# Kernel tuning notes

Hardware: AMD Instinct MI355X
Metric: run time of the kernel (lower is better)

Reference implementation:

```python
import jax, jax.numpy as jnp
import numpy as np

HEADS = 56
OUT = 32       # hidden_channels (per-head out dim)
N_FEAT = 128
N_CLASS = 2
N_NODES = 20000
N_EDGES = 100000
N_GRAPHS = 50
EPS_BN = 1e-5


def _gat_conv(x, W, att_src, att_dst, bias, src, dst, n, concat):
    # x: [n, in]; W: [in, H*O]; att_*: [H, O]
    h = (x @ W).reshape(n, HEADS, OUT)                     # [n, H, O]
    a_s = jnp.sum(h * att_src, axis=-1)                    # [n, H]
    a_d = jnp.sum(h * att_dst, axis=-1)                    # [n, H]
    e = jax.nn.leaky_relu(a_s[src] + a_d[dst], 0.2)        # [E, H]
    m = jax.ops.segment_max(e, dst, num_segments=n)        # per-dst max
    ex = jnp.exp(e - m[dst])
    den = jax.ops.segment_sum(ex, dst, num_segments=n)
    alpha = ex / den[dst]                                  # segment softmax over incoming edges
    msg = h[src] * alpha[:, :, None]                       # [E, H, O]
    out = jax.ops.segment_sum(msg, dst, num_segments=n)    # [n, H, O]
    if concat:
        return out.reshape(n, HEADS * OUT) + bias
    return out.mean(axis=1) + bias


def _bn_eval(x, gamma, beta, mean, var):
    return (x - mean) * jax.lax.rsqrt(var + EPS_BN) * gamma + beta


def setup_inputs() -> dict:
    key = jax.random.key(0)
    ks = jax.random.split(key, 20)
    d1 = HEADS * OUT
    inp = {
        'x': jax.random.normal(ks[0], (N_NODES, N_FEAT), jnp.float32),
        'edge_index': jax.random.randint(ks[1], (2, N_EDGES), 0, N_NODES, jnp.int32),
        'batch': jnp.sort(jax.random.randint(ks[2], (N_NODES,), 0, N_GRAPHS, jnp.int32)),
        'W1': jax.random.normal(ks[3], (N_FEAT, d1), jnp.float32) * (1.0 / np.sqrt(N_FEAT)),
        'att_src1': jax.random.normal(ks[4], (HEADS, OUT), jnp.float32) * 0.1,
        'att_dst1': jax.random.normal(ks[5], (HEADS, OUT), jnp.float32) * 0.1,
        'b1': jnp.zeros((d1,), jnp.float32),
        'bn1_g': jnp.ones((d1,), jnp.float32),
        'bn1_b': jnp.zeros((d1,), jnp.float32),
        'bn1_m': jax.random.normal(ks[6], (d1,), jnp.float32) * 0.1,
        'bn1_v': jax.random.uniform(ks[7], (d1,), jnp.float32) + 0.5,
        'W2': jax.random.normal(ks[8], (d1, d1), jnp.float32) * (1.0 / np.sqrt(d1)),
        'att_src2': jax.random.normal(ks[9], (HEADS, OUT), jnp.float32) * 0.1,
        'att_dst2': jax.random.normal(ks[10], (HEADS, OUT), jnp.float32) * 0.1,
        'b2': jnp.zeros((OUT,), jnp.float32),
        'bn2_g': jnp.ones((OUT,), jnp.float32),
        'bn2_b': jnp.zeros((OUT,), jnp.float32),
        'bn2_m': jax.random.normal(ks[11], (OUT,), jnp.float32) * 0.1,
        'bn2_v': jax.random.uniform(ks[12], (OUT,), jnp.float32) + 0.5,
        'lin_w': jax.random.normal(ks[13], (OUT, N_CLASS), jnp.float32) * (1.0 / np.sqrt(OUT)),
        'lin_b': jnp.zeros((N_CLASS,), jnp.float32),
    }
    return inp


def reference(x, edge_index, batch, W1, att_src1, att_dst1, b1, bn1_g, bn1_b, bn1_m, bn1_v,
              W2, att_src2, att_dst2, b2, bn2_g, bn2_b, bn2_m, bn2_v, lin_w, lin_b):
    n = x.shape[0]
    loop = jnp.arange(n, dtype=edge_index.dtype)
    src = jnp.concatenate([edge_index[0], loop])   # PyG GATConv add_self_loops=True
    dst = jnp.concatenate([edge_index[1], loop])

    h = jax.nn.elu(_gat_conv(x, W1, att_src1, att_dst1, b1, src, dst, n, concat=True))
    h = _bn_eval(h, bn1_g, bn1_b, bn1_m, bn1_v)
    # dropout p=0.5 is identity in eval
    h = _gat_conv(h, W2, att_src2, att_dst2, b2, src, dst, n, concat=False)
    h = _bn_eval(h, bn2_g, bn2_b, bn2_m, bn2_v)

    sums = jax.ops.segment_sum(h, batch, num_segments=N_GRAPHS)
    cnt = jax.ops.segment_sum(jnp.ones((n, 1), h.dtype), batch, num_segments=N_GRAPHS)
    pooled = sums / jnp.maximum(cnt, 1.0)          # global_mean_pool
    return pooled @ lin_w + lin_b
```

## Files before the change

kernel.cpp:

```cpp
#include <hip/hip_runtime.h>
#include <hip/hip_bf16.h>
#include <hip/hip_fp8.h>
#include <cstdint>
#include <cstddef>

#define NN     20000
#define NF     128
#define NH     56
#define OC     32
#define DD1    1792
#define NE     100000
#define ETOT   120000
#define NG     50
#define EPS_BN 1e-5f
#define GRP    16
#define EB     16

typedef __bf16 bf16x8 __attribute__((ext_vector_type(8)));
typedef float  floatx4 __attribute__((ext_vector_type(4)));
typedef float  floatx2 __attribute__((ext_vector_type(2)));
typedef unsigned int u32;
typedef __attribute__((address_space(1))) u32 gu32;
typedef __attribute__((address_space(3))) u32 lu32;

__device__ __forceinline__ void async_copy16(void* lds, const void* g) {
    __builtin_amdgcn_global_load_lds((gu32*)const_cast<void*>(g), (lu32*)lds, 16, 0, 0);
}

__device__ __forceinline__ void dec_fp8x4(u32 u, float* v) {
#if __has_builtin(__builtin_amdgcn_cvt_pk_f32_fp8)
    floatx2 lo = __builtin_amdgcn_cvt_pk_f32_fp8(u, false);
    floatx2 hi = __builtin_amdgcn_cvt_pk_f32_fp8(u, true);
    v[0] = lo[0]; v[1] = lo[1]; v[2] = hi[0]; v[3] = hi[1];
#else
    #pragma unroll
    for (int b = 0; b < 4; ++b) {
        __hip_fp8_e4m3 t;
        t.__x = (u >> (8 * b)) & 0xff;
        v[b] = (float)t;
    }
#endif
}

__device__ __forceinline__ void fma_fp8x4(u32 u, float a, float* acc) {
    float v[4];
    dec_fp8x4(u, v);
    #pragma unroll
    for (int b = 0; b < 4; ++b) acc[b] += a * v[b];
}

template <int CTRL>
__device__ __forceinline__ float dpp_row_add(float x) {
    int v = __builtin_amdgcn_mov_dpp(__float_as_int(x), CTRL, 0xf, 0xf, true);
    return x + __int_as_float(v);
}
__device__ __forceinline__ float dpp_add16(float x) {
    x = dpp_row_add<0x128>(x);
    x = dpp_row_add<0x124>(x);
    x = dpp_row_add<78>(x);
    x = dpp_row_add<177>(x);
    return x;
}

__global__ __launch_bounds__(256) void cast_bf16_kernel(const float* __restrict__ in,
                                                        __hip_bfloat16* __restrict__ out, int n) {
    int i = blockIdx.x * 256 + threadIdx.x;
    if (i < n) out[i] = __float2bfloat16(in[i]);
}

__global__ __launch_bounds__(256) void transpose_cast_kernel(const float* __restrict__ in,
                                                             __hip_bfloat16* __restrict__ out,
                                                             int R, int C) {
    __shared__ float tile[32][33];
    int c0 = blockIdx.x * 32, r0 = blockIdx.y * 32;
    int tx = threadIdx.x & 31, ty = threadIdx.x >> 5;
    #pragma unroll
    for (int i = 0; i < 32; i += 8) {
        int r = r0 + ty + i, c = c0 + tx;
        if (r < R && c < C) tile[ty + i][tx] = in[(size_t)r * C + c];
    }
    __syncthreads();
    #pragma unroll
    for (int i = 0; i < 32; i += 8) {
        int c = c0 + ty + i, r = r0 + tx;
        if (c < C && r < R) out[(size_t)c * R + r] = __float2bfloat16(tile[tx][ty + i]);
    }
}

__global__ __launch_bounds__(256) void hist_kernel(const int* __restrict__ ei, int* __restrict__ deg) {
    int i = blockIdx.x * 256 + threadIdx.x;
    if (i >= ETOT) return;
    int dst = (i < NE) ? ei[NE + i] : (i - NE);
    atomicAdd(&deg[dst], 1);
}

__global__ __launch_bounds__(1024) void scan_kernel(const int* __restrict__ deg,
                                                    int* __restrict__ rowptr,
                                                    int* __restrict__ cursor) {
    __shared__ int buf[1024];
    int t = threadIdx.x;
    const int CH = (NN + 1023) >> 10;
    int base = t * CH;
    int s = 0;
    for (int j = 0; j < CH; ++j) { int idx = base + j; if (idx < NN) s += deg[idx]; }
    buf[t] = s;
    __syncthreads();
    for (int off = 1; off < 1024; off <<= 1) {
        int v = (t >= off) ? buf[t - off] : 0;
        __syncthreads();
        buf[t] += v;
        __syncthreads();
    }
    int run = buf[t] - s;
    for (int j = 0; j < CH; ++j) {
        int idx = base + j;
        if (idx < NN) { rowptr[idx] = run; cursor[idx] = run; run += deg[idx]; }
    }
    if (t == 1023) rowptr[NN] = buf[1023];
}

__global__ __launch_bounds__(256) void scatter_kernel(const int* __restrict__ ei,
                                                      int* __restrict__ cursor,
                                                      int* __restrict__ csr_src) {
    int i = blockIdx.x * 256 + threadIdx.x;
    if (i >= ETOT) return;
    int s, d;
    if (i < NE) { s = ei[i]; d = ei[NE + i]; } else { s = i - NE; d = i - NE; }
    int pos = atomicAdd(&cursor[d], 1);
    csr_src[pos] = s;
}

__global__ __launch_bounds__(512, 2) void gemm_192(const __hip_bfloat16* __restrict__ A,
                                                   const __hip_bfloat16* __restrict__ Bt,
                                                   unsigned char* __restrict__ C8,
                                                   const float* __restrict__ att_src,
                                                   const float* __restrict__ att_dst,
                                                   float* __restrict__ as_,
                                                   float* __restrict__ ad_,
                                                   int M, int N, int K) {
    __shared__ __align__(16) unsigned short lds[2][28672];
    const int tid  = threadIdx.x;
    const int lane = tid & 63, wave = tid >> 6;
    const int wm = wave >> 2, wn = wave & 3;

    const int nbx = N >> 8;
    const int nby = (M + 191) / 192;
    const int nwg = nbx * nby;
    const int q = nwg >> 3, r = nwg & 7;
    const int xcd = blockIdx.x & 7, bidx = blockIdx.x >> 3;
    const int wg = (xcd < r ? xcd * (q + 1) : r * (q + 1) + (xcd - r) * q) + bidx;
    const int by = wg / nbx, bx = wg - by * nbx;
    const int m0 = by * 192, n0 = bx << 8;

    const int NT = K >> 6;

    const int qq = lane >> 4, rr = lane & 15;

    auto stageA = [&](int kt, int b) {
        #pragma unroll
        for (int i = 0; i < 3; ++i) {
            int slot = i * 512 + tid;
            int row = slot >> 3, pch = slot & 7;
            int lc = pch ^ (row & 7);
            int gr = m0 + row; if (gr > M - 1) gr = M - 1;
            async_copy16(&lds[b][slot * 8], A + (size_t)gr * K + (kt << 6) + lc * 8);
        }
    };
    auto stageB = [&](int kt, int b) {
        #pragma unroll
        for (int i = 0; i < 4; ++i) {
            int slot = i * 512 + tid;
            int row = slot >> 3, pch = slot & 7;
            int lc = pch ^ (row & 7);
            async_copy16(&lds[b][12288 + slot * 8], Bt + (size_t)(n0 + row) * K + (kt << 6) + lc * 8);
        }
    };

    floatx4 zero = {0.f, 0.f, 0.f, 0.f};
    floatx4 acc[6][4];
    #pragma unroll
    for (int i = 0; i < 6; ++i)
        #pragma unroll
        for (int jj = 0; jj < 4; ++jj) acc[i][jj] = zero;

    bf16x8 aF[3][2], bA[2][2], bB[2][2];

    auto loadA = [&](int b, int mg) {
        #pragma unroll
        for (int mf = 0; mf < 3; ++mf)
            #pragma unroll
            for (int s = 0; s < 2; ++s) {
                int row = wm * 96 + mg * 48 + mf * 16 + rr;
                int pch = (s * 4 + qq) ^ (row & 7);
                aF[mf][s] = *(const bf16x8*)&lds[b][row * 64 + pch * 8];
            }
    };
    auto loadB = [&](int b, bf16x8 (&bF)[2][2], int ng) {
        #pragma unroll
        for (int nf = 0; nf < 2; ++nf)
            #pragma unroll
            for (int s = 0; s < 2; ++s) {
                int row = wn * 64 + (ng * 2 + nf) * 16 + rr;
                int pch = (s * 4 + qq) ^ (row & 7);
                bF[nf][s] = *(const bf16x8*)&lds[b][12288 + row * 64 + pch * 8];
            }
    };
    auto mfmaQ = [&](int mg, int ng, bf16x8 (&bF)[2][2]) {
        #pragma unroll
        for (int mf = 0; mf < 3; ++mf)
            #pragma unroll
            for (int nf = 0; nf < 2; ++nf)
                #pragma unroll
                for (int s = 0; s < 2; ++s)
                    acc[mg * 3 + mf][ng * 2 + nf] = __builtin_amdgcn_mfma_f32_16x16x32_bf16(
                        aF[mf][s], bF[nf][s], acc[mg * 3 + mf][ng * 2 + nf], 0, 0, 0);
    };

#define SB0 __builtin_amdgcn_sched_barrier(0)
#define GBAR do { SB0; __builtin_amdgcn_s_barrier(); SB0; } while (0)

    stageB(0, 0); stageA(0, 0);
    stageB(1, 1); stageA(1, 1);
    SB0;
    asm volatile("s_waitcnt vmcnt(7)" ::: "memory");
    GBAR;

    for (int t = 0; t < NT; ++t) {
        const int p = t & 1;
        int tp = t + 2; while (tp >= NT) tp -= 2;

        loadA(p, 0); loadB(p, bA, 0);
        GBAR;
        __builtin_amdgcn_s_setprio(1);
        mfmaQ(0, 0, bA);
        __builtin_amdgcn_s_setprio(0);
        GBAR;

        loadB(p, bB, 1);
        stageB(tp, p);
        GBAR;
        __builtin_amdgcn_s_setprio(1);
        mfmaQ(0, 1, bB);
        __builtin_amdgcn_s_setprio(0);
        GBAR;

        loadA(p, 1);
        stageA(tp, p);
        SB0;
        asm volatile("s_waitcnt vmcnt(7)" ::: "memory");
        GBAR;
        __builtin_amdgcn_s_setprio(1);
        mfmaQ(1, 1, bB);
        mfmaQ(1, 0, bA);
        __builtin_amdgcn_s_setprio(0);
        GBAR;
    }
#undef GBAR
#undef SB0

    #pragma unroll
    for (int mt = 0; mt < 6; ++mt) {
        #pragma unroll
        for (int r4 = 0; r4 < 4; ++r4) {
            int rowc = m0 + wm * 96 + mt * 16 + (lane >> 4) * 4 + r4;
            if (rowc < M) {
                float v0 = acc[mt][0][r4], v1 = acc[mt][1][r4];
                float v2 = acc[mt][2][r4], v3 = acc[mt][3][r4];
                unsigned char q8[4];
#if __has_builtin(__builtin_amdgcn_cvt_pk_fp8_f32)
                u32 p01 = (u32)__builtin_amdgcn_cvt_pk_fp8_f32(v0, v1, 0, false);
                u32 p23 = (u32)__builtin_amdgcn_cvt_pk_fp8_f32(v2, v3, 0, false);
                q8[0] = p01 & 0xff; q8[1] = (p01 >> 8) & 0xff;
                q8[2] = p23 & 0xff; q8[3] = (p23 >> 8) & 0xff;
#else
                { __hip_fp8_e4m3 t0(v0), t1(v1), t2(v2), t3(v3);
                  q8[0] = t0.__x; q8[1] = t1.__x; q8[2] = t2.__x; q8[3] = t3.__x; }
#endif
                #pragma unroll
                for (int nt = 0; nt < 4; ++nt) {
                    int col = n0 + wn * 64 + nt * 16 + (lane & 15);
                    C8[(size_t)rowc * N + col] = q8[nt];
                }
            }
        }
    }

    {
        const int li = lane & 15;
        const int h0 = bx * 8 + wn * 2;
        float ws00 = att_src[(h0)     * OC + li],      ws01 = att_src[(h0)     * OC + 16 + li];
        float ws10 = att_src[(h0 + 1) * OC + li],      ws11 = att_src[(h0 + 1) * OC + 16 + li];
        float wd00 = att_dst[(h0)     * OC + li],      wd01 = att_dst[(h0)     * OC + 16 + li];
        float wd10 = att_dst[(h0 + 1) * OC + li],      wd11 = att_dst[(h0 + 1) * OC + 16 + li];
        #pragma unroll
        for (int mt = 0; mt < 6; ++mt) {
            #pragma unroll
            for (int r4 = 0; r4 < 4; ++r4) {
                float s0 = dpp_add16(acc[mt][0][r4] * ws00 + acc[mt][1][r4] * ws01);
                float s1 = dpp_add16(acc[mt][2][r4] * ws10 + acc[mt][3][r4] * ws11);
                float d0 = dpp_add16(acc[mt][0][r4] * wd00 + acc[mt][1][r4] * wd01);
                float d1 = dpp_add16(acc[mt][2][r4] * wd10 + acc[mt][3][r4] * wd11);
                int rowc = m0 + wm * 96 + mt * 16 + (lane >> 4) * 4 + r4;
                if (li == 0 && rowc < M) {
                    as_[(size_t)rowc * NH + h0]     = s0;
                    as_[(size_t)rowc * NH + h0 + 1] = s1;
                    ad_[(size_t)rowc * NH + h0]     = d0;
                    ad_[(size_t)rowc * NH + h0 + 1] = d1;
                }
            }
        }
    }
}

template <int LAYER>
__device__ __forceinline__ void flush_node(float* acc, float den, int cur, int f, int lane,
                                           const float* __restrict__ bias,
                                           const float* __restrict__ bng,
                                           const float* __restrict__ bnb,
                                           const float* __restrict__ bnm,
                                           const float* __restrict__ bnv,
                                           void* __restrict__ outp) {
    float inv = 1.f / den;
    #pragma unroll
    for (int k = 0; k < 4; ++k) acc[k] *= inv;

    if constexpr (LAYER == 1) {
        int d0 = f * 256 + lane * 4;
        u32 r01, r23;
        {
            float v0 = acc[0] + bias[d0 + 0];
            float v1 = acc[1] + bias[d0 + 1];
            float v2 = acc[2] + bias[d0 + 2];
            float v3 = acc[3] + bias[d0 + 3];
            v0 = v0 > 0.f ? v0 : expm1f(v0);
            v1 = v1 > 0.f ? v1 : expm1f(v1);
            v2 = v2 > 0.f ? v2 : expm1f(v2);
            v3 = v3 > 0.f ? v3 : expm1f(v3);
            v0 = (v0 - bnm[d0 + 0]) * rsqrtf(bnv[d0 + 0] + EPS_BN) * bng[d0 + 0] + bnb[d0 + 0];
            v1 = (v1 - bnm[d0 + 1]) * rsqrtf(bnv[d0 + 1] + EPS_BN) * bng[d0 + 1] + bnb[d0 + 1];
            v2 = (v2 - bnm[d0 + 2]) * rsqrtf(bnv[d0 + 2] + EPS_BN) * bng[d0 + 2] + bnb[d0 + 2];
            v3 = (v3 - bnm[d0 + 3]) * rsqrtf(bnv[d0 + 3] + EPS_BN) * bng[d0 + 3] + bnb[d0 + 3];
            __hip_bfloat16 b0 = __float2bfloat16(v0), b1 = __float2bfloat16(v1);
            __hip_bfloat16 b2 = __float2bfloat16(v2), b3 = __float2bfloat16(v3);
            r01 = (u32)*(unsigned short*)&b0 | ((u32)*(unsigned short*)&b1 << 16);
            r23 = (u32)*(unsigned short*)&b2 | ((u32)*(unsigned short*)&b3 << 16);
        }
        uint2 pk; pk.x = r01; pk.y = r23;
        *(uint2*)((__hip_bfloat16*)outp + (size_t)cur * DD1 + d0) = pk;
    } else {
        #pragma unroll
        for (int k = 0; k < 4; ++k) {
            acc[k] += __shfl_xor(acc[k], 8, 64);
            acc[k] += __shfl_xor(acc[k], 16, 64);
            acc[k] += __shfl_xor(acc[k], 32, 64);
        }
        if (lane < 8) {
            floatx4 pk;
            #pragma unroll
            for (int k = 0; k < 4; ++k) pk[k] = acc[k] * (1.f / NH);
            *(floatx4*)((float*)outp + ((size_t)cur * 7 + f) * OC + lane * 4) = pk;
        }
    }
    acc[0] = acc[1] = acc[2] = acc[3] = 0.f;
}

template <int LAYER>
__global__ __launch_bounds__(256) void attn_aggregate(const int* __restrict__ rowptr,
                                                      const int* __restrict__ csr_src,
                                                      const float* __restrict__ as_,
                                                      const float* __restrict__ ad_,
                                                      const unsigned char* __restrict__ h8,
                                                      const float* __restrict__ bias,
                                                      const float* __restrict__ bng,
                                                      const float* __restrict__ bnb,
                                                      const float* __restrict__ bnm,
                                                      const float* __restrict__ bnv,
                                                      void* __restrict__ outp) {
    const int wv = threadIdx.x >> 6, lane = threadIdx.x & 63;
    const int w = blockIdx.x * 4 + wv;
    const int NWAVES = 7 * (NN / GRP);
    if (w >= NWAVES) return;
    const int f  = w % 7;
    const int g  = w / 7;
    const int n0 = g * GRP;
    const int off  = f * 256 + lane * 4;
    const int head = f * 8 + (lane >> 3);

    const int e0 = rowptr[n0], e1 = rowptr[n0 + GRP];
    int cur = n0;
    int bound = rowptr[n0 + 1];
    float adv = ad_[(size_t)cur * NH + head];

    float acc[4] = {0.f, 0.f, 0.f, 0.f};
    float m = -1e30f, den = 0.f;

    for (int e = e0; e < e1; e += EB) {
        u32   hv[EB];
        float sv[EB];
        #pragma unroll
        for (int i = 0; i < EB; ++i) {
            int idx = (e + i < e1) ? e + i : e1 - 1;
            int s = csr_src[idx];
            hv[i] = *(const u32*)(h8 + (size_t)s * DD1 + off);
            sv[i] = as_[(size_t)s * NH + head];
        }
        #pragma unroll
        for (int i = 0; i < EB; ++i) {
            if (e + i >= e1) break;
            if (e + i >= bound) {
                flush_node<LAYER>(acc, den, cur, f, lane, bias, bng, bnb, bnm, bnv, outp);
                ++cur;
                bound = rowptr[cur + 1];
                adv = ad_[(size_t)cur * NH + head];
                m = -1e30f; den = 0.f;
            }
            float lr = sv[i] + adv;
            lr = lr > 0.f ? lr : 0.2f * lr;
            float wgt;
            if (lr > m) {
                float scale = __expf(m - lr);
                den = den * scale + 1.f;
                #pragma unroll
                for (int k = 0; k < 4; ++k) acc[k] *= scale;
                m = lr;
                wgt = 1.f;
            } else {
                wgt = __expf(lr - m);
                den += wgt;
            }
            fma_fp8x4(hv[i], wgt, acc);
        }
    }
    flush_node<LAYER>(acc, den, cur, f, lane, bias, bng, bnb, bnm, bnv, outp);
}

__global__ __launch_bounds__(256) void pool_kernel(const float* __restrict__ h2part,
                                                   const int* __restrict__ batch,
                                                   float* __restrict__ sums,
                                                   float* __restrict__ cnt) {
    __shared__ float red[4][OC];
    const int g = blockIdx.x >> 3, c = blockIdx.x & 7;
    const int t = threadIdx.x;
    const int ch = t & 31, nl = t >> 5;
    int lo = 0, hi = NN;
    while (lo < hi) { int mid = (lo + hi) >> 1; if (batch[mid] < g) lo = mid + 1; else hi = mid; }
    const int s = lo;
    hi = NN;
    while (lo < hi) { int mid = (lo + hi) >> 1; if (batch[mid] <= g) lo = mid + 1; else hi = mid; }
    const int e = lo;
    const int len = e - s;
    const int n0 = s + (len * c) / 8;
    const int n1 = s + (len * (c + 1)) / 8;
    float acc = 0.f;
    for (int n = n0 + nl; n < n1; n += 8) {
        const float* p = h2part + (size_t)n * 7 * OC + ch;
        float a = 0.f;
        #pragma unroll
        for (int f = 0; f < 7; ++f) a += p[f * OC];
        acc += a;
    }
    acc += __shfl_xor(acc, 32, 64);
    if ((t & 32) == 0) red[t >> 6][ch] = acc;
    __syncthreads();
    if (t < OC) {
        float total = red[0][t] + red[1][t] + red[2][t] + red[3][t];
        atomicAdd(&sums[g * OC + t], total);
    }
    if (t == 0 && c == 0) cnt[g] = (float)len;
}

__global__ __launch_bounds__(128) void final_kernel(const float* __restrict__ sums,
                                                    const float* __restrict__ cnt,
                                                    const float* __restrict__ b2,
                                                    const float* __restrict__ bn2g,
                                                    const float* __restrict__ bn2b,
                                                    const float* __restrict__ bn2m,
                                                    const float* __restrict__ bn2v,
                                                    const float* __restrict__ lin_w,
                                                    const float* __restrict__ lin_b,
                                                    float* __restrict__ out) {
    int t = threadIdx.x;
    if (t >= NG * 2) return;
    int g = t >> 1, c = t & 1;
    float invc = 1.f / fmaxf(cnt[g], 1.f);
    float acc = lin_b[c];
    #pragma unroll
    for (int o = 0; o < OC; ++o) {
        float pooled = sums[g * OC + o] * invc + b2[o];
        float v = (pooled - bn2m[o]) * rsqrtf(bn2v[o] + EPS_BN) * bn2g[o] + bn2b[o];
        acc += v * lin_w[o * 2 + c];
    }
    out[t] = acc;
}

extern "C" void kernel_launch(void* const* d_in, const int* in_sizes, int n_in,
                              void* d_out, int out_size, void* d_ws, size_t ws_size,
                              hipStream_t stream) {
    const float* x    = (const float*)d_in[0];
    const int*   ei   = (const int*)d_in[1];
    const int*   bat  = (const int*)d_in[2];
    const float* W1   = (const float*)d_in[3];
    const float* at_s1 = (const float*)d_in[4];
    const float* at_d1 = (const float*)d_in[5];
    const float* b1   = (const float*)d_in[6];
    const float* bn1g = (const float*)d_in[7];
    const float* bn1b = (const float*)d_in[8];
    const float* bn1m = (const float*)d_in[9];
    const float* bn1v = (const float*)d_in[10];
    const float* W2   = (const float*)d_in[11];
    const float* at_s2 = (const float*)d_in[12];
    const float* at_d2 = (const float*)d_in[13];
    const float* b2   = (const float*)d_in[14];
    const float* bn2g = (const float*)d_in[15];
    const float* bn2b = (const float*)d_in[16];
    const float* bn2m = (const float*)d_in[17];
    const float* bn2v = (const float*)d_in[18];
    const float* linw = (const float*)d_in[19];
    const float* linb = (const float*)d_in[20];
    float* out = (float*)d_out;

    char* wsp = (char*)d_ws;
    auto alloc = [&](size_t bytes) -> void* {
        void* p = (void*)wsp;
        wsp += (bytes + 255) & ~(size_t)255;
        return p;
    };
    unsigned char*  h8  = (unsigned char*)alloc((size_t)NN * DD1);
    __hip_bfloat16* h1p = (__hip_bfloat16*)alloc((size_t)NN * DD1 * 2);
    __hip_bfloat16* xb  = (__hip_bfloat16*)alloc((size_t)NN * NF * 2);
    __hip_bfloat16* w1t = (__hip_bfloat16*)alloc((size_t)DD1 * NF * 2);
    __hip_bfloat16* w2t = (__hip_bfloat16*)alloc((size_t)DD1 * DD1 * 2);
    float* asb   = (float*)alloc((size_t)NN * NH * 4);
    float* adb   = (float*)alloc((size_t)NN * NH * 4);
    int*   deg   = (int*)alloc((size_t)NN * 4);
    int*   rowp  = (int*)alloc((size_t)(NN + 1) * 4);
    int*   curs  = (int*)alloc((size_t)NN * 4);
    int*   csr   = (int*)alloc((size_t)ETOT * 4);
    float* h2part = (float*)alloc((size_t)NN * 7 * OC * 4);
    float* sums  = (float*)alloc((size_t)(NG * OC + NG) * 4);
    float* cnt   = sums + NG * OC;

    hipMemsetAsync(deg, 0, (size_t)NN * 4, stream);
    hipMemsetAsync(sums, 0, (size_t)(NG * OC + NG) * 4, stream);

    cast_bf16_kernel<<<(NN * NF + 255) / 256, 256, 0, stream>>>(x, xb, NN * NF);
    transpose_cast_kernel<<<dim3(DD1 / 32, NF / 32), 256, 0, stream>>>(W1, w1t, NF, DD1);
    transpose_cast_kernel<<<dim3(DD1 / 32, DD1 / 32), 256, 0, stream>>>(W2, w2t, DD1, DD1);
    hist_kernel<<<(ETOT + 255) / 256, 256, 0, stream>>>(ei, deg);
    scan_kernel<<<1, 1024, 0, stream>>>(deg, rowp, curs);
    scatter_kernel<<<(ETOT + 255) / 256, 256, 0, stream>>>(ei, curs, csr);

    const int AGG_BLOCKS = (7 * (NN / GRP) + 3) / 4;
    const int NBY192 = (NN + 191) / 192;
    const int GEMM_BLOCKS = NBY192 * (DD1 / 256);

    gemm_192<<<GEMM_BLOCKS, 512, 0, stream>>>(xb, w1t, h8, at_s1, at_d1, asb, adb, NN, DD1, NF);
    attn_aggregate<1><<<AGG_BLOCKS, 256, 0, stream>>>(rowp, csr, asb, adb, h8, b1, bn1g, bn1b, bn1m, bn1v, (void*)h1p);

    gemm_192<<<GEMM_BLOCKS, 512, 0, stream>>>(h1p, w2t, h8, at_s2, at_d2, asb, adb, NN, DD1, DD1);
    attn_aggregate<2><<<AGG_BLOCKS, 256, 0, stream>>>(rowp, csr, asb, adb, h8, b2, bn2g, bn2b, bn2m, bn2v, (void*)h2part);

    pool_kernel<<<NG * 8, 256, 0, stream>>>(h2part, bat, sums, cnt);
    final_kernel<<<1, 128, 0, stream>>>(sums, cnt, b2, bn2g, bn2b, bn2m, bn2v, linw, linb, out);
}
```

Before: 521.8 us.

## Run layer-2 GEMM in FP8 with scaled weights and FP8 layer-1 output

Layer-1 aggregation now writes its activations as FP8 e4m3 instead of bf16. W2 is transposed and quantized to FP8 with a x16 scale. A new gemm_fp8 kernel uses 16x16x32 fp8 MFMA with a 128-wide K tile and undoes the scale in the epilogue. This halves the bytes of the largest GEMM's operands and the intermediate activation traffic, and it uses the higher-throughput FP8 matrix path. The cost is reduced precision in the second layer's inputs and weights, which risks accuracy loss.

New measurement: 517.7 us. Within noise of the previous version (-0.8%).

```diff
diff --git a/kernel.cpp b/kernel.cpp
--- a/kernel.cpp
+++ b/kernel.cpp
@@ -15,6 +15,7 @@
 #define EPS_BN 1e-5f
 #define GRP    16
 #define EB     16
+#define W2SCL  16.0f
 
 typedef __bf16 bf16x8 __attribute__((ext_vector_type(8)));
 typedef float  floatx4 __attribute__((ext_vector_type(4)));
@@ -42,6 +43,17 @@
 #endif
 }
 
+__device__ __forceinline__ u32 enc_fp8x4(float v0, float v1, float v2, float v3) {
+#if __has_builtin(__builtin_amdgcn_cvt_pk_fp8_f32)
+    u32 p01 = (u32)__builtin_amdgcn_cvt_pk_fp8_f32(v0, v1, 0, false);
+    u32 p23 = (u32)__builtin_amdgcn_cvt_pk_fp8_f32(v2, v3, 0, false);
+    return (p01 & 0xffff) | (p23 << 16);
+#else
+    __hip_fp8_e4m3 t0(v0), t1(v1), t2(v2), t3(v3);
+    return (u32)t0.__x | ((u32)t1.__x << 8) | ((u32)t2.__x << 16) | ((u32)t3.__x << 24);
+#endif
+}
+
 __device__ __forceinline__ void fma_fp8x4(u32 u, float a, float* acc) {
     float v[4];
     dec_fp8x4(u, v);
@@ -84,6 +96,28 @@
     for (int i = 0; i < 32; i += 8) {
         int c = c0 + ty + i, r = r0 + tx;
         if (c < C && r < R) out[(size_t)c * R + r] = __float2bfloat16(tile[tx][ty + i]);
+    }
+}
+
+__global__ __launch_bounds__(256) void transpose_fp8_kernel(const float* __restrict__ in,
+                                                            unsigned char* __restrict__ out,
+                                                            int R, int C) {
+    __shared__ float tile[32][33];
+    int c0 = blockIdx.x * 32, r0 = blockIdx.y * 32;
+    int tx = threadIdx.x & 31, ty = threadIdx.x >> 5;
+    #pragma unroll
+    for (int i = 0; i < 32; i += 8) {
+        int r = r0 + ty + i, c = c0 + tx;
+        if (r < R && c < C) tile[ty + i][tx] = in[(size_t)r * C + c];
+    }
+    __syncthreads();
+    #pragma unroll
+    for (int i = 0; i < 32; i += 8) {
+        int c = c0 + ty + i, r = r0 + tx;
+        if (c < C && r < R) {
+            __hip_fp8_e4m3 t(tile[tx][ty + i] * W2SCL);
+            out[(size_t)c * R + r] = t.__x;
+        }
     }
 }
 
@@ -264,18 +298,9 @@
         for (int r4 = 0; r4 < 4; ++r4) {
             int rowc = m0 + wm * 96 + mt * 16 + (lane >> 4) * 4 + r4;
             if (rowc < M) {
-                float v0 = acc[mt][0][r4], v1 = acc[mt][1][r4];
-                float v2 = acc[mt][2][r4], v3 = acc[mt][3][r4];
-                unsigned char q8[4];
-#if __has_builtin(__builtin_amdgcn_cvt_pk_fp8_f32)
-                u32 p01 = (u32)__builtin_amdgcn_cvt_pk_fp8_f32(v0, v1, 0, false);
-                u32 p23 = (u32)__builtin_amdgcn_cvt_pk_fp8_f32(v2, v3, 0, false);
-                q8[0] = p01 & 0xff; q8[1] = (p01 >> 8) & 0xff;
-                q8[2] = p23 & 0xff; q8[3] = (p23 >> 8) & 0xff;
-#else
-                { __hip_fp8_e4m3 t0(v0), t1(v1), t2(v2), t3(v3);
-                  q8[0] = t0.__x; q8[1] = t1.__x; q8[2] = t2.__x; q8[3] = t3.__x; }
-#endif
+                u32 word = enc_fp8x4(acc[mt][0][r4], acc[mt][1][r4], acc[mt][2][r4], acc[mt][3][r4]);
+                unsigned char q8[4] = { (unsigned char)(word & 0xff), (unsigned char)((word >> 8) & 0xff),
+                                        (unsigned char)((word >> 16) & 0xff), (unsigned char)(word >> 24) };
                 #pragma unroll
                 for (int nt = 0; nt < 4; ++nt) {
                     int col = n0 + wn * 64 + nt * 16 + (lane & 15);
@@ -312,6 +337,182 @@
     }
 }
 
+__global__ __launch_bounds__(512, 2) void gemm_fp8(const unsigned char* __restrict__ A,
+                                                   const unsigned char* __restrict__ Bt,
+                                                   unsigned char* __restrict__ C8,
+                                                   const float* __restrict__ att_src,
+                                                   const float* __restrict__ att_dst,
+                                                   float* __restrict__ as_,
+                                                   float* __restrict__ ad_,
+                                                   int M, int N, int K) {
+    __shared__ __align__(16) unsigned char lds8[2][57344];
+    const int tid  = threadIdx.x;
+    const int lane = tid & 63, wave = tid >> 6;
+    const int wm = wave >> 2, wn = wave & 3;
+
+    const int nbx = N >> 8;
+    const int nby = (M + 191) / 192;
+    const int nwg = nbx * nby;
+    const int q = nwg >> 3, r = nwg & 7;
+    const int xcd = blockIdx.x & 7, bidx = blockIdx.x >> 3;
+    const int wg = (xcd < r ? xcd * (q + 1) : r * (q + 1) + (xcd - r) * q) + bidx;
+    const int by = wg / nbx, bx = wg - by * nbx;
+    const int m0 = by * 192, n0 = bx << 8;
+
+    const int NT = K >> 7;
+
+    const int qq = lane >> 4, rr = lane & 15;
+
+    auto stageA = [&](int kt, int b) {
+        #pragma unroll
+        for (int i = 0; i < 3; ++i) {
+            int slot = i * 512 + tid;
+            int row = slot >> 3, pch = slot & 7;
+            int lc = pch ^ (row & 7);
+            int gr = m0 + row; if (gr > M - 1) gr = M - 1;
+            async_copy16(&lds8[b][slot * 16], A + (size_t)gr * K + (kt << 7) + lc * 16);
+        }
+    };
+    auto stageB = [&](int kt, int b) {
+        #pragma unroll
+        for (int i = 0; i < 4; ++i) {
+            int slot = i * 512 + tid;
+            int row = slot >> 3, pch = slot & 7;
+            int lc = pch ^ (row & 7);
+            async_copy16(&lds8[b][24576 + slot * 16], Bt + (size_t)(n0 + row) * K + (kt << 7) + lc * 16);
+        }
+    };
+
+    floatx4 zero = {0.f, 0.f, 0.f, 0.f};
+    floatx4 acc[6][4];
+    #pragma unroll
+    for (int i = 0; i < 6; ++i)
+        #pragma unroll
+        for (int jj = 0; jj < 4; ++jj) acc[i][jj] = zero;
+
+    long aF[3][4], bA[2][4], bB[2][4];
+
+    auto loadA = [&](int b, int mg) {
+        #pragma unroll
+        for (int mf = 0; mf < 3; ++mf)
+            #pragma unroll
+            for (int s = 0; s < 4; ++s) {
+                int row = wm * 96 + mg * 48 + mf * 16 + rr;
+                int ch = (2 * s + (qq >> 1)) ^ (row & 7);
+                aF[mf][s] = *(const long*)&lds8[b][row * 128 + ch * 16 + (qq & 1) * 8];
+            }
+    };
+    auto loadB = [&](int b, long (&bF)[2][4], int ng) {
+        #pragma unroll
+        for (int nf = 0; nf < 2; ++nf)
+            #pragma unroll
+            for (int s = 0; s < 4; ++s) {
+                int row = wn * 64 + (ng * 2 + nf) * 16 + rr;
+                int ch = (2 * s + (qq >> 1)) ^ (row & 7);
+                bF[nf][s] = *(const long*)&lds8[b][24576 + row * 128 + ch * 16 + (qq & 1) * 8];
+            }
+    };
+    auto mfmaQ = [&](int mg, int ng, long (&bF)[2][4]) {
+        #pragma unroll
+        for (int mf = 0; mf < 3; ++mf)
+            #pragma unroll
+            for (int nf = 0; nf < 2; ++nf)
+                #pragma unroll
+                for (int s = 0; s < 4; ++s)
+                    acc[mg * 3 + mf][ng * 2 + nf] = __builtin_amdgcn_mfma_f32_16x16x32_fp8_fp8(
+                        aF[mf][s], bF[nf][s], acc[mg * 3 + mf][ng * 2 + nf], 0, 0, 0);
+    };
+
+#define SB0 __builtin_amdgcn_sched_barrier(0)
+#define GBAR do { SB0; __builtin_amdgcn_s_barrier(); SB0; } while (0)
+
+    stageB(0, 0); stageA(0, 0);
+    stageB(1, 1); stageA(1, 1);
+    SB0;
+    asm volatile("s_waitcnt vmcnt(7)" ::: "memory");
+    GBAR;
+
+    for (int t = 0; t < NT; ++t) {
+        const int p = t & 1;
+        int tp = t + 2; while (tp >= NT) tp -= 2;
+
+        loadA(p, 0); loadB(p, bA, 0);
+        GBAR;
+        __builtin_amdgcn_s_setprio(1);
+        mfmaQ(0, 0, bA);
+        __builtin_amdgcn_s_setprio(0);
+        GBAR;
+
+        loadB(p, bB, 1);
+        stageB(tp, p);
+        GBAR;
+        __builtin_amdgcn_s_setprio(1);
+        mfmaQ(0, 1, bB);
+        __builtin_amdgcn_s_setprio(0);
+        GBAR;
+
+        loadA(p, 1);
+        stageA(tp, p);
+        SB0;
+        asm volatile("s_waitcnt vmcnt(7)" ::: "memory");
+        GBAR;
+        __builtin_amdgcn_s_setprio(1);
+        mfmaQ(1, 1, bB);
+        mfmaQ(1, 0, bA);
+        __builtin_amdgcn_s_setprio(0);
+        GBAR;
+    }
+#undef GBAR
+#undef SB0
+
+    const float scl = 1.0f / W2SCL;
+
+    #pragma unroll
+    for (int mt = 0; mt < 6; ++mt) {
+        #pragma unroll
+        for (int r4 = 0; r4 < 4; ++r4) {
+            int rowc = m0 + wm * 96 + mt * 16 + (lane >> 4) * 4 + r4;
+            if (rowc < M) {
+                u32 word = enc_fp8x4(acc[mt][0][r4] * scl, acc[mt][1][r4] * scl,
+                                     acc[mt][2][r4] * scl, acc[mt][3][r4] * scl);
+                unsigned char q8[4] = { (unsigned char)(word & 0xff), (unsigned char)((word >> 8) & 0xff),
+                                        (unsigned char)((word >> 16) & 0xff), (unsigned char)(word >> 24) };
+                #pragma unroll
+                for (int nt = 0; nt < 4; ++nt) {
+                    int col = n0 + wn * 64 + nt * 16 + (lane & 15);
+                    C8[(size_t)rowc * N + col] = q8[nt];
+                }
+            }
+        }
+    }
+
+    {
+        const int li = lane & 15;
+        const int h0 = bx * 8 + wn * 2;
+        float ws00 = att_src[(h0)     * OC + li] * scl,  ws01 = att_src[(h0)     * OC + 16 + li] * scl;
+        float ws10 = att_src[(h0 + 1) * OC + li] * scl,  ws11 = att_src[(h0 + 1) * OC + 16 + li] * scl;
+        float wd00 = att_dst[(h0)     * OC + li] * scl,  wd01 = att_dst[(h0)     * OC + 16 + li] * scl;
+        float wd10 = att_dst[(h0 + 1) * OC + li] * scl,  wd11 = att_dst[(h0 + 1) * OC + 16 + li] * scl;
+        #pragma unroll
+        for (int mt = 0; mt < 6; ++mt) {
+            #pragma unroll
+            for (int r4 = 0; r4 < 4; ++r4) {
+                float s0 = dpp_add16(acc[mt][0][r4] * ws00 + acc[mt][1][r4] * ws01);
+                float s1 = dpp_add16(acc[mt][2][r4] * ws10 + acc[mt][3][r4] * ws11);
+                float d0 = dpp_add16(acc[mt][0][r4] * wd00 + acc[mt][1][r4] * wd01);
+                float d1 = dpp_add16(acc[mt][2][r4] * wd10 + acc[mt][3][r4] * wd11);
+                int rowc = m0 + wm * 96 + mt * 16 + (lane >> 4) * 4 + r4;
+                if (li == 0 && rowc < M) {
+                    as_[(size_t)rowc * NH + h0]     = s0;
+                    as_[(size_t)rowc * NH + h0 + 1] = s1;
+                    ad_[(size_t)rowc * NH + h0]     = d0;
+                    ad_[(size_t)rowc * NH + h0 + 1] = d1;
+                }
+            }
+        }
+    }
+}
+
 template <int LAYER>
 __device__ __forceinline__ void flush_node(float* acc, float den, int cur, int f, int lane,
                                            const float* __restrict__ bias,
@@ -326,27 +527,20 @@
 
     if constexpr (LAYER == 1) {
         int d0 = f * 256 + lane * 4;
-        u32 r01, r23;
-        {
-            float v0 = acc[0] + bias[d0 + 0];
-            float v1 = acc[1] + bias[d0 + 1];
-            float v2 = acc[2] + bias[d0 + 2];
-            float v3 = acc[3] + bias[d0 + 3];
-            v0 = v0 > 0.f ? v0 : expm1f(v0);
-            v1 = v1 > 0.f ? v1 : expm1f(v1);
-            v2 = v2 > 0.f ? v2 : expm1f(v2);
-            v3 = v3 > 0.f ? v3 : expm1f(v3);
-            v0 = (v0 - bnm[d0 + 0]) * rsqrtf(bnv[d0 + 0] + EPS_BN) * bng[d0 + 0] + bnb[d0 + 0];
-            v1 = (v1 - bnm[d0 + 1]) * rsqrtf(bnv[d0 + 1] + EPS_BN) * bng[d0 + 1] + bnb[d0 + 1];
-            v2 = (v2 - bnm[d0 + 2]) * rsqrtf(bnv[d0 + 2] + EPS_BN) * bng[d0 + 2] + bnb[d0 + 2];
-            v3 = (v3 - bnm[d0 + 3]) * rsqrtf(bnv[d0 + 3] + EPS_BN) * bng[d0 + 3] + bnb[d0 + 3];
-            __hip_bfloat16 b0 = __float2bfloat16(v0), b1 = __float2bfloat16(v1);
-            __hip_bfloat16 b2 = __float2bfloat16(v2), b3 = __float2bfloat16(v3);
-            r01 = (u32)*(unsigned short*)&b0 | ((u32)*(unsigned short*)&b1 << 16);
-            r23 = (u32)*(unsigned short*)&b2 | ((u32)*(unsigned short*)&b3 << 16);
-        }
-        uint2 pk; pk.x = r01; pk.y = r23;
-        *(uint2*)((__hip_bfloat16*)outp + (size_t)cur * DD1 + d0) = pk;
+        float v0 = acc[0] + bias[d0 + 0];
+        float v1 = acc[1] + bias[d0 + 1];
+        float v2 = acc[2] + bias[d0 + 2];
+        float v3 = acc[3] + bias[d0 + 3];
+        v0 = v0 > 0.f ? v0 : expm1f(v0);
+        v1 = v1 > 0.f ? v1 : expm1f(v1);
+        v2 = v2 > 0.f ? v2 : expm1f(v2);
+        v3 = v3 > 0.f ? v3 : expm1f(v3);
+        v0 = (v0 - bnm[d0 + 0]) * rsqrtf(bnv[d0 + 0] + EPS_BN) * bng[d0 + 0] + bnb[d0 + 0];
+        v1 = (v1 - bnm[d0 + 1]) * rsqrtf(bnv[d0 + 1] + EPS_BN) * bng[d0 + 1] + bnb[d0 + 1];
+        v2 = (v2 - bnm[d0 + 2]) * rsqrtf(bnv[d0 + 2] + EPS_BN) * bng[d0 + 2] + bnb[d0 + 2];
+        v3 = (v3 - bnm[d0 + 3]) * rsqrtf(bnv[d0 + 3] + EPS_BN) * bng[d0 + 3] + bnb[d0 + 3];
+        u32 word = enc_fp8x4(v0, v1, v2, v3);
+        *(u32*)((unsigned char*)outp + (size_t)cur * DD1 + d0) = word;
     } else {
         #pragma unroll
         for (int k = 0; k < 4; ++k) {
@@ -525,11 +719,11 @@
         wsp += (bytes + 255) & ~(size_t)255;
         return p;
     };
-    unsigned char*  h8  = (unsigned char*)alloc((size_t)NN * DD1);
-    __hip_bfloat16* h1p = (__hip_bfloat16*)alloc((size_t)NN * DD1 * 2);
-    __hip_bfloat16* xb  = (__hip_bfloat16*)alloc((size_t)NN * NF * 2);
-    __hip_bfloat16* w1t = (__hip_bfloat16*)alloc((size_t)DD1 * NF * 2);
-    __hip_bfloat16* w2t = (__hip_bfloat16*)alloc((size_t)DD1 * DD1 * 2);
+    unsigned char*  h8   = (unsigned char*)alloc((size_t)NN * DD1);
+    unsigned char*  h1p  = (unsigned char*)alloc((size_t)NN * DD1);
+    __hip_bfloat16* xb   = (__hip_bfloat16*)alloc((size_t)NN * NF * 2);
+    __hip_bfloat16* w1t  = (__hip_bfloat16*)alloc((size_t)DD1 * NF * 2);
+    unsigned char*  w2t8 = (unsigned char*)alloc((size_t)DD1 * DD1);
     float* asb   = (float*)alloc((size_t)NN * NH * 4);
     float* adb   = (float*)alloc((size_t)NN * NH * 4);
     int*   deg   = (int*)alloc((size_t)NN * 4);
@@ -545,7 +739,7 @@
 
     cast_bf16_kernel<<<(NN * NF + 255) / 256, 256, 0, stream>>>(x, xb, NN * NF);
     transpose_cast_kernel<<<dim3(DD1 / 32, NF / 32), 256, 0, stream>>>(W1, w1t, NF, DD1);
-    transpose_cast_kernel<<<dim3(DD1 / 32, DD1 / 32), 256, 0, stream>>>(W2, w2t, DD1, DD1);
+    transpose_fp8_kernel<<<dim3(DD1 / 32, DD1 / 32), 256, 0, stream>>>(W2, w2t8, DD1, DD1);
     hist_kernel<<<(ETOT + 255) / 256, 256, 0, stream>>>(ei, deg);
     scan_kernel<<<1, 1024, 0, stream>>>(deg, rowp, curs);
     scatter_kernel<<<(ETOT + 255) / 256, 256, 0, stream>>>(ei, curs, csr);
@@ -557,7 +751,7 @@
     gemm_192<<<GEMM_BLOCKS, 512, 0, stream>>>(xb, w1t, h8, at_s1, at_d1, asb, adb, NN, DD1, NF);
     attn_aggregate<1><<<AGG_BLOCKS, 256, 0, stream>>>(rowp, csr, asb, adb, h8, b1, bn1g, bn1b, bn1m, bn1v, (void*)h1p);
 
-    gemm_192<<<GEMM_BLOCKS, 512, 0, stream>>>(h1p, w2t, h8, at_s2, at_d2, asb, adb, NN, DD1, DD1);
+    gemm_fp8<<<GEMM_BLOCKS, 512, 0, stream>>>(h1p, w2t8, h8, at_s2, at_d2, asb, adb, NN, DD1, DD1);
     attn_aggregate<2><<<AGG_BLOCKS, 256, 0, stream>>>(rowp, csr, asb, adb, h8, b2, bn2g, bn2b, bn2m, bn2v, (void*)h2part);
 
     pool_kernel<<<NG * 8, 256, 0, stream>>>(h2part, bat, sums, cnt);
```

## Switch both GEMMs to FP8 MFMA with scaled weights and FP8 activations

Applied to the files above, without the earlier changes.

Converts x, W1 and W2 to FP8 e4m3, with per-weight scale factors folded back into the epilogue and attention coefficients. The GEMM now runs 16x16x32 fp8 MFMAs over K-tiles of 128 bytes. The layer-1 aggregate output is stored as FP8 instead of bf16, halving activation traffic into the second GEMM. The cost is extra quantization error in inputs, weights and hidden activations, and K=128 for layer 1 gives only a single tile iteration.

After: 501.4 us. -3.9%, faster.

```diff
diff --git a/kernel.cpp b/kernel.cpp
--- a/kernel.cpp
+++ b/kernel.cpp
@@ -15,16 +15,24 @@
 #define EPS_BN 1e-5f
 #define GRP    16
 #define EB     16
+#define W1SCL  8.0f
+#define W2SCL  16.0f
 
 typedef __bf16 bf16x8 __attribute__((ext_vector_type(8)));
 typedef float  floatx4 __attribute__((ext_vector_type(4)));
 typedef float  floatx2 __attribute__((ext_vector_type(2)));
+typedef long   longx2  __attribute__((ext_vector_type(2)));
 typedef unsigned int u32;
 typedef __attribute__((address_space(1))) u32 gu32;
 typedef __attribute__((address_space(3))) u32 lu32;
 
 __device__ __forceinline__ void async_copy16(void* lds, const void* g) {
     __builtin_amdgcn_global_load_lds((gu32*)const_cast<void*>(g), (lu32*)lds, 16, 0, 0);
+}
+
+__device__ __forceinline__ longx2 ld_lds16(const unsigned char* p) {
+    bf16x8 raw = *(const bf16x8*)p;
+    return __builtin_bit_cast(longx2, raw);
 }
 
 __device__ __forceinline__ void dec_fp8x4(u32 u, float* v) {
@@ -42,6 +50,17 @@
 #endif
 }
 
+__device__ __forceinline__ u32 enc_fp8x4(float v0, float v1, float v2, float v3) {
+#if __has_builtin(__builtin_amdgcn_cvt_pk_fp8_f32)
+    u32 p01 = (u32)__builtin_amdgcn_cvt_pk_fp8_f32(v0, v1, 0, false);
+    u32 p23 = (u32)__builtin_amdgcn_cvt_pk_fp8_f32(v2, v3, 0, false);
+    return (p01 & 0xffff) | (p23 << 16);
+#else
+    __hip_fp8_e4m3 t0(v0), t1(v1), t2(v2), t3(v3);
+    return (u32)t0.__x | ((u32)t1.__x << 8) | ((u32)t2.__x << 16) | ((u32)t3.__x << 24);
+#endif
+}
+
 __device__ __forceinline__ void fma_fp8x4(u32 u, float a, float* acc) {
     float v[4];
     dec_fp8x4(u, v);
@@ -62,15 +81,18 @@
     return x;
 }
 
-__global__ __launch_bounds__(256) void cast_bf16_kernel(const float* __restrict__ in,
-                                                        __hip_bfloat16* __restrict__ out, int n) {
+__global__ __launch_bounds__(256) void cast_fp8_kernel(const float* __restrict__ in,
+                                                       unsigned char* __restrict__ out, int n) {
     int i = blockIdx.x * 256 + threadIdx.x;
-    if (i < n) out[i] = __float2bfloat16(in[i]);
-}
-
-__global__ __launch_bounds__(256) void transpose_cast_kernel(const float* __restrict__ in,
-                                                             __hip_bfloat16* __restrict__ out,
-                                                             int R, int C) {
+    if (i < n) {
+        __hip_fp8_e4m3 t(in[i]);
+        out[i] = t.__x;
+    }
+}
+
+__global__ __launch_bounds__(256) void transpose_fp8_kernel(const float* __restrict__ in,
+                                                            unsigned char* __restrict__ out,
+                                                            int R, int C, float scale) {
     __shared__ float tile[32][33];
     int c0 = blockIdx.x * 32, r0 = blockIdx.y * 32;
     int tx = threadIdx.x & 31, ty = threadIdx.x >> 5;
@@ -83,7 +105,10 @@
     #pragma unroll
     for (int i = 0; i < 32; i += 8) {
         int c = c0 + ty + i, r = r0 + tx;
-        if (c < C && r < R) out[(size_t)c * R + r] = __float2bfloat16(tile[tx][ty + i]);
+        if (c < C && r < R) {
+            __hip_fp8_e4m3 t(tile[tx][ty + i] * scale);
+            out[(size_t)c * R + r] = t.__x;
+        }
     }
 }
 
@@ -130,15 +155,15 @@
     csr_src[pos] = s;
 }
 
-__global__ __launch_bounds__(512, 2) void gemm_192(const __hip_bfloat16* __restrict__ A,
-                                                   const __hip_bfloat16* __restrict__ Bt,
+__global__ __launch_bounds__(512, 2) void gemm_fp8(const unsigned char* __restrict__ A,
+                                                   const unsigned char* __restrict__ Bt,
                                                    unsigned char* __restrict__ C8,
                                                    const float* __restrict__ att_src,
                                                    const float* __restrict__ att_dst,
                                                    float* __restrict__ as_,
                                                    float* __restrict__ ad_,
-                                                   int M, int N, int K) {
-    __shared__ __align__(16) unsigned short lds[2][28672];
+                                                   int M, int N, int K, float inv_scale) {
+    __shared__ __align__(16) unsigned char lds8[2][57344];
     const int tid  = threadIdx.x;
     const int lane = tid & 63, wave = tid >> 6;
     const int wm = wave >> 2, wn = wave & 3;
@@ -152,27 +177,29 @@
     const int by = wg / nbx, bx = wg - by * nbx;
     const int m0 = by * 192, n0 = bx << 8;
 
-    const int NT = K >> 6;
+    const int NT = K >> 7;
 
     const int qq = lane >> 4, rr = lane & 15;
 
     auto stageA = [&](int kt, int b) {
+        if (kt > NT - 1) kt = NT - 1;
         #pragma unroll
         for (int i = 0; i < 3; ++i) {
             int slot = i * 512 + tid;
             int row = slot >> 3, pch = slot & 7;
             int lc = pch ^ (row & 7);
             int gr = m0 + row; if (gr > M - 1) gr = M - 1;
-            async_copy16(&lds[b][slot * 8], A + (size_t)gr * K + (kt << 6) + lc * 8);
+            async_copy16(&lds8[b][slot * 16], A + (size_t)gr * K + (kt << 7) + lc * 16);
         }
     };
     auto stageB = [&](int kt, int b) {
+        if (kt > NT - 1) kt = NT - 1;
         #pragma unroll
         for (int i = 0; i < 4; ++i) {
             int slot = i * 512 + tid;
             int row = slot >> 3, pch = slot & 7;
             int lc = pch ^ (row & 7);
-            async_copy16(&lds[b][12288 + slot * 8], Bt + (size_t)(n0 + row) * K + (kt << 6) + lc * 8);
+            async_copy16(&lds8[b][24576 + slot * 16], Bt + (size_t)(n0 + row) * K + (kt << 7) + lc * 16);
         }
     };
 
@@ -183,37 +210,39 @@
         #pragma unroll
         for (int jj = 0; jj < 4; ++jj) acc[i][jj] = zero;
 
-    bf16x8 aF[3][2], bA[2][2], bB[2][2];
+    longx2 aF[3][2], bA[2][2], bB[2][2];
 
     auto loadA = [&](int b, int mg) {
         #pragma unroll
         for (int mf = 0; mf < 3; ++mf)
             #pragma unroll
-            for (int s = 0; s < 2; ++s) {
+            for (int j = 0; j < 2; ++j) {
                 int row = wm * 96 + mg * 48 + mf * 16 + rr;
-                int pch = (s * 4 + qq) ^ (row & 7);
-                aF[mf][s] = *(const bf16x8*)&lds[b][row * 64 + pch * 8];
+                int ch = ((j << 2) + qq) ^ (row & 7);
+                aF[mf][j] = ld_lds16(&lds8[b][row * 128 + ch * 16]);
             }
     };
-    auto loadB = [&](int b, bf16x8 (&bF)[2][2], int ng) {
+    auto loadB = [&](int b, longx2 (&bF)[2][2], int ng) {
         #pragma unroll
         for (int nf = 0; nf < 2; ++nf)
             #pragma unroll
-            for (int s = 0; s < 2; ++s) {
+            for (int j = 0; j < 2; ++j) {
                 int row = wn * 64 + (ng * 2 + nf) * 16 + rr;
-                int pch = (s * 4 + qq) ^ (row & 7);
-                bF[nf][s] = *(const bf16x8*)&lds[b][12288 + row * 64 + pch * 8];
+                int ch = ((j << 2) + qq) ^ (row & 7);
+                bF[nf][j] = ld_lds16(&lds8[b][24576 + row * 128 + ch * 16]);
             }
     };
-    auto mfmaQ = [&](int mg, int ng, bf16x8 (&bF)[2][2]) {
+    auto mfmaQ = [&](int mg, int ng, longx2 (&bF)[2][2]) {
         #pragma unroll
         for (int mf = 0; mf < 3; ++mf)
             #pragma unroll
             for (int nf = 0; nf < 2; ++nf)
                 #pragma unroll
-                for (int s = 0; s < 2; ++s)
-                    acc[mg * 3 + mf][ng * 2 + nf] = __builtin_amdgcn_mfma_f32_16x16x32_bf16(
-                        aF[mf][s], bF[nf][s], acc[mg * 3 + mf][ng * 2 + nf], 0, 0, 0);
+                for (int j = 0; j < 2; ++j)
+                    #pragma unroll
+                    for (int h = 0; h < 2; ++h)
+                        acc[mg * 3 + mf][ng * 2 + nf] = __builtin_amdgcn_mfma_f32_16x16x32_fp8_fp8(
+                            aF[mf][j][h], bF[nf][j][h], acc[mg * 3 + mf][ng * 2 + nf], 0, 0, 0);
     };
 
 #define SB0 __builtin_amdgcn_sched_barrier(0)
@@ -228,6 +257,7 @@
     for (int t = 0; t < NT; ++t) {
         const int p = t & 1;
         int tp = t + 2; while (tp >= NT) tp -= 2;
+        if (tp < 0) tp = 0;
 
         loadA(p, 0); loadB(p, bA, 0);
         GBAR;
@@ -258,24 +288,18 @@
 #undef GBAR
 #undef SB0
 
+    const float scl = inv_scale;
+
     #pragma unroll
     for (int mt = 0; mt < 6; ++mt) {
         #pragma unroll
         for (int r4 = 0; r4 < 4; ++r4) {
             int rowc = m0 + wm * 96 + mt * 16 + (lane >> 4) * 4 + r4;
             if (rowc < M) {
-                float v0 = acc[mt][0][r4], v1 = acc[mt][1][r4];
-                float v2 = acc[mt][2][r4], v3 = acc[mt][3][r4];
-                unsigned char q8[4];
-#if __has_builtin(__builtin_amdgcn_cvt_pk_fp8_f32)
-                u32 p01 = (u32)__builtin_amdgcn_cvt_pk_fp8_f32(v0, v1, 0, false);
-                u32 p23 = (u32)__builtin_amdgcn_cvt_pk_fp8_f32(v2, v3, 0, false);
-                q8[0] = p01 & 0xff; q8[1] = (p01 >> 8) & 0xff;
-                q8[2] = p23 & 0xff; q8[3] = (p23 >> 8) & 0xff;
-#else
-                { __hip_fp8_e4m3 t0(v0), t1(v1), t2(v2), t3(v3);
-                  q8[0] = t0.__x; q8[1] = t1.__x; q8[2] = t2.__x; q8[3] = t3.__x; }
-#endif
+                u32 word = enc_fp8x4(acc[mt][0][r4] * scl, acc[mt][1][r4] * scl,
+                                     acc[mt][2][r4] * scl, acc[mt][3][r4] * scl);
+                unsigned char q8[4] = { (unsigned char)(word & 0xff), (unsigned char)((word >> 8) & 0xff),
+                                        (unsigned char)((word >> 16) & 0xff), (unsigned char)(word >> 24) };
                 #pragma unroll
                 for (int nt = 0; nt < 4; ++nt) {
                     int col = n0 + wn * 64 + nt * 16 + (lane & 15);
@@ -288,10 +312,10 @@
     {
         const int li = lane & 15;
         const int h0 = bx * 8 + wn * 2;
-        float ws00 = att_src[(h0)     * OC + li],      ws01 = att_src[(h0)     * OC + 16 + li];
-        float ws10 = att_src[(h0 + 1) * OC + li],      ws11 = att_src[(h0 + 1) * OC + 16 + li];
-        float wd00 = att_dst[(h0)     * OC + li],      wd01 = att_dst[(h0)     * OC + 16 + li];
-        float wd10 = att_dst[(h0 + 1) * OC + li],      wd11 = att_dst[(h0 + 1) * OC + 16 + li];
+        float ws00 = att_src[(h0)     * OC + li] * scl,  ws01 = att_src[(h0)     * OC + 16 + li] * scl;
+        float ws10 = att_src[(h0 + 1) * OC + li] * scl,  ws11 = att_src[(h0 + 1) * OC + 16 + li] * scl;
+        float wd00 = att_dst[(h0)     * OC + li] * scl,  wd01 = att_dst[(h0)     * OC + 16 + li] * scl;
+        float wd10 = att_dst[(h0 + 1) * OC + li] * scl,  wd11 = att_dst[(h0 + 1) * OC + 16 + li] * scl;
         #pragma unroll
         for (int mt = 0; mt < 6; ++mt) {
             #pragma unroll
@@ -326,27 +350,20 @@
 
     if constexpr (LAYER == 1) {
         int d0 = f * 256 + lane * 4;
-        u32 r01, r23;
-        {
-            float v0 = acc[0] + bias[d0 + 0];
-            float v1 = acc[1] + bias[d0 + 1];
-            float v2 = acc[2] + bias[d0 + 2];
-            float v3 = acc[3] + bias[d0 + 3];
-            v0 = v0 > 0.f ? v0 : expm1f(v0);
-            v1 = v1 > 0.f ? v1 : expm1f(v1);
-            v2 = v2 > 0.f ? v2 : expm1f(v2);
-            v3 = v3 > 0.f ? v3 : expm1f(v3);
-            v0 = (v0 - bnm[d0 + 0]) * rsqrtf(bnv[d0 + 0] + EPS_BN) * bng[d0 + 0] + bnb[d0 + 0];
-            v1 = (v1 - bnm[d0 + 1]) * rsqrtf(bnv[d0 + 1] + EPS_BN) * bng[d0 + 1] + bnb[d0 + 1];
-            v2 = (v2 - bnm[d0 + 2]) * rsqrtf(bnv[d0 + 2] + EPS_BN) * bng[d0 + 2] + bnb[d0 + 2];
-            v3 = (v3 - bnm[d0 + 3]) * rsqrtf(bnv[d0 + 3] + EPS_BN) * bng[d0 + 3] + bnb[d0 + 3];
-            __hip_bfloat16 b0 = __float2bfloat16(v0), b1 = __float2bfloat16(v1);
-            __hip_bfloat16 b2 = __float2bfloat16(v2), b3 = __float2bfloat16(v3);
-            r01 = (u32)*(unsigned short*)&b0 | ((u32)*(unsigned short*)&b1 << 16);
-            r23 = (u32)*(unsigned short*)&b2 | ((u32)*(unsigned short*)&b3 << 16);
-        }
-        uint2 pk; pk.x = r01; pk.y = r23;
-        *(uint2*)((__hip_bfloat16*)outp + (size_t)cur * DD1 + d0) = pk;
+        float v0 = acc[0] + bias[d0 + 0];
+        float v1 = acc[1] + bias[d0 + 1];
+        float v2 = acc[2] + bias[d0 + 2];
+        float v3 = acc[3] + bias[d0 + 3];
+        v0 = v0 > 0.f ? v0 : expm1f(v0);
+        v1 = v1 > 0.f ? v1 : expm1f(v1);
+        v2 = v2 > 0.f ? v2 : expm1f(v2);
+        v3 = v3 > 0.f ? v3 : expm1f(v3);
+        v0 = (v0 - bnm[d0 + 0]) * rsqrtf(bnv[d0 + 0] + EPS_BN) * bng[d0 + 0] + bnb[d0 + 0];
+        v1 = (v1 - bnm[d0 + 1]) * rsqrtf(bnv[d0 + 1] + EPS_BN) * bng[d0 + 1] + bnb[d0 + 1];
+        v2 = (v2 - bnm[d0 + 2]) * rsqrtf(bnv[d0 + 2] + EPS_BN) * bng[d0 + 2] + bnb[d0 + 2];
+        v3 = (v3 - bnm[d0 + 3]) * rsqrtf(bnv[d0 + 3] + EPS_BN) * bng[d0 + 3] + bnb[d0 + 3];
+        u32 word = enc_fp8x4(v0, v1, v2, v3);
+        *(u32*)((unsigned char*)outp + (size_t)cur * DD1 + d0) = word;
     } else {
         #pragma unroll
         for (int k = 0; k < 4; ++k) {
@@ -525,11 +542,11 @@
         wsp += (bytes + 255) & ~(size_t)255;
         return p;
     };
-    unsigned char*  h8  = (unsigned char*)alloc((size_t)NN * DD1);
-    __hip_bfloat16* h1p = (__hip_bfloat16*)alloc((size_t)NN * DD1 * 2);
-    __hip_bfloat16* xb  = (__hip_bfloat16*)alloc((size_t)NN * NF * 2);
-    __hip_bfloat16* w1t = (__hip_bfloat16*)alloc((size_t)DD1 * NF * 2);
-    __hip_bfloat16* w2t = (__hip_bfloat16*)alloc((size_t)DD1 * DD1 * 2);
+    unsigned char*  h8   = (unsigned char*)alloc((size_t)NN * DD1);
+    unsigned char*  h1p  = (unsigned char*)alloc((size_t)NN * DD1);
+    unsigned char*  xb8  = (unsigned char*)alloc((size_t)NN * NF);
+    unsigned char*  w1t8 = (unsigned char*)alloc((size_t)DD1 * NF);
+    unsigned char*  w2t8 = (unsigned char*)alloc((size_t)DD1 * DD1);
     float* asb   = (float*)alloc((size_t)NN * NH * 4);
     float* adb   = (float*)alloc((size_t)NN * NH * 4);
     int*   deg   = (int*)alloc((size_t)NN * 4);
@@ -543,9 +560,9 @@
     hipMemsetAsync(deg, 0, (size_t)NN * 4, stream);
     hipMemsetAsync(sums, 0, (size_t)(NG * OC + NG) * 4, stream);
 
-    cast_bf16_kernel<<<(NN * NF + 255) / 256, 256, 0, stream>>>(x, xb, NN * NF);
-    transpose_cast_kernel<<<dim3(DD1 / 32, NF / 32), 256, 0, stream>>>(W1, w1t, NF, DD1);
-    transpose_cast_kernel<<<dim3(DD1 / 32, DD1 / 32), 256, 0, stream>>>(W2, w2t, DD1, DD1);
+    cast_fp8_kernel<<<(NN * NF + 255) / 256, 256, 0, stream>>>(x, xb8, NN * NF);
+    transpose_fp8_kernel<<<dim3(DD1 / 32, NF / 32), 256, 0, stream>>>(W1, w1t8, NF, DD1, W1SCL);
+    transpose_fp8_kernel<<<dim3(DD1 / 32, DD1 / 32), 256, 0, stream>>>(W2, w2t8, DD1, DD1, W2SCL);
     hist_kernel<<<(ETOT + 255) / 256, 256, 0, stream>>>(ei, deg);
     scan_kernel<<<1, 1024, 0, stream>>>(deg, rowp, curs);
     scatter_kernel<<<(ETOT + 255) / 256, 256, 0, stream>>>(ei, curs, csr);
@@ -554,10 +571,10 @@
     const int NBY192 = (NN + 191) / 192;
     const int GEMM_BLOCKS = NBY192 * (DD1 / 256);
 
-    gemm_192<<<GEMM_BLOCKS, 512, 0, stream>>>(xb, w1t, h8, at_s1, at_d1, asb, adb, NN, DD1, NF);
+    gemm_fp8<<<GEMM_BLOCKS, 512, 0, stream>>>(xb8, w1t8, h8, at_s1, at_d1, asb, adb, NN, DD1, NF, 1.0f / W1SCL);
     attn_aggregate<1><<<AGG_BLOCKS, 256, 0, stream>>>(rowp, csr, asb, adb, h8, b1, bn1g, bn1b, bn1m, bn1v, (void*)h1p);
 
-    gemm_192<<<GEMM_BLOCKS, 512, 0, stream>>>(h1p, w2t, h8, at_s2, at_d2, asb, adb, NN, DD1, DD1);
+    gemm_fp8<<<GEMM_BLOCKS, 512, 0, stream>>>(h1p, w2t8, h8, at_s2, at_d2, asb, adb, NN, DD1, DD1, 1.0f / W2SCL);
     attn_aggregate<2><<<AGG_BLOCKS, 256, 0, stream>>>(rowp, csr, asb, adb, h8, b2, bn2g, bn2b, bn2m, bn2v, (void*)h2part);
 
     pool_kernel<<<NG * 8, 256, 0, stream>>>(h2part, bat, sums, cnt);
```
